# Kernel optimization log

Measured on AMD Instinct MI355X. Metric: run time of the kernel, lower is better.

## Reference

```python
import jax, jax.numpy as jnp
import numpy as np

ALPHA = 32.0
LN_EPS = 1e-5

def _cdist(a, b):
    # a: [C, M, K], b: [C, N, K] -> [C, M, N] euclidean distances
    d2 = (jnp.sum(a * a, -1)[:, :, None]
          + jnp.sum(b * b, -1)[:, None, :]
          - 2.0 * jnp.einsum('cmk,cnk->cmn', a, b))
    return jnp.sqrt(jnp.maximum(d2, 1e-12))

def setup_inputs() -> dict:
    key = jax.random.key(0)
    k1, k2 = jax.random.split(key)
    B, D, H, W, C = 8, 16, 28, 28, 256
    CN, SS = 128, 28 * 28
    x = jax.random.normal(k1, (B, D, H, W, C), dtype=jnp.float32)
    ln_weight = jnp.ones((C,), dtype=jnp.float32)
    ln_bias = jnp.zeros((C,), dtype=jnp.float32)
    cluster_center = jax.random.uniform(k2, (C, CN, SS), dtype=jnp.float32)
    return {"x": x, "ln_weight": ln_weight, "ln_bias": ln_bias,
            "cluster_center": cluster_center}

def reference(x, ln_weight, ln_bias, cluster_center):
    B, D, H, W, C = x.shape
    CN = cluster_center.shape[1]
    # LayerNorm over last dim (feature_dim)
    mu = jnp.mean(x, -1, keepdims=True)
    var = jnp.mean(jnp.square(x - mu), -1, keepdims=True)
    xn = (x - mu) * jax.lax.rsqrt(var + LN_EPS) * ln_weight + ln_bias
    # B D H W C -> C (B D) (H W)
    x_re = jnp.transpose(xn, (4, 0, 1, 2, 3)).reshape(C, B * D, H * W)
    soft_assign = _cdist(x_re, cluster_center)          # [C, B*D, CN]
    # C (B D) CN -> B D C CN
    x_distance = jnp.transpose(soft_assign.reshape(C, B, D, CN), (1, 2, 0, 3))
    # NegSoftAssign: exp(-alpha*(x - min)) normalized == softmax(-alpha*x)
    x_distance_assign = jax.nn.softmax(-ALPHA * x_distance, axis=-1)
    cluster_dist = _cdist(cluster_center, cluster_center)  # [C, CN, CN]
    return (x_distance, x_distance_assign, cluster_dist)
```

## Files before the change

### kernel.cpp

```cpp
#include <hip/hip_runtime.h>
#include <hip/hip_bf16.h>
#include <math.h>

#define C_DIM 256
#define BD    128
#define HW    784
#define CN    128
#define KPAD  832
#define KTILES 26

typedef short bf16x8 __attribute__((ext_vector_type(8)));
typedef float f32x4 __attribute__((ext_vector_type(4)));

__device__ inline ushort f2b(float f) {
  unsigned u = __float_as_uint(f);
  unsigned r = (u + 0x7FFFu + ((u >> 16) & 1u)) >> 16;
  return (ushort)r;
}

__global__ __launch_bounds__(256, 4) void prep_kernel(
    const float* __restrict__ x, const float* __restrict__ lnw,
    const float* __restrict__ lnb, const float* __restrict__ cc,
    ushort* __restrict__ xre, ushort* __restrict__ ccb) {
  __shared__ __align__(16) ushort btile[256 * 64];
  const int t = threadIdx.x, bid = blockIdx.x;
  const int w = t >> 6, lane = t & 63;
  const int q = lane >> 4, l = lane & 15;

  if (bid < 2048) {
    const int c = bid >> 3;
    const int r = (bid & 7) * 16 + w * 4 + q;
    const float4* src = (const float4*)(cc + ((size_t)c * CN + r) * HW);
    ushort* dst = ccb + ((size_t)c * CN + r) * KPAD;
    float4 v[13];
#pragma unroll
    for (int i = 0; i < 13; ++i) {
      if (i < 12 || l < 4) v[i] = src[i * 16 + l];
    }
#pragma unroll
    for (int i = 0; i < 13; ++i) {
      if (i < 12 || l < 4) {
        ushort4 o;
        o.x = f2b(v[i].x); o.y = f2b(v[i].y);
        o.z = f2b(v[i].z); o.w = f2b(v[i].w);
        *(ushort4*)(dst + (i * 16 + l) * 4) = o;
      }
    }
    if (l < 12) *(ushort4*)(dst + 784 + l * 4) = make_ushort4(0, 0, 0, 0);
    return;
  }

  const int idx = bid - 2048;
  const int bx = idx % 13;
  const int bd = idx / 13;
  const int hw0 = bx * 64;
  const bool last = (bx == 12);
  const int ngroups = last ? 1 : 4;
  const int rpw = ngroups * 4;
  const int xr2 = (l & 12) | ((l & 3) << 4);
  if (last) {
    int xf = ((t >> 2) & 12) ^ ((t & 12) << 2);
    for (int r = 16; r < 64; r += 4)
      *(ushort4*)&btile[t * 64 + (r ^ xf)] = make_ushort4(0, 0, 0, 0);
  }
  float4 wv[4], bv[4];
#pragma unroll
  for (int s = 0; s < 4; ++s) {
    wv[s] = *(const float4*)(lnw + s * 64 + l * 4);
    bv[s] = *(const float4*)(lnb + s * 64 + l * 4);
  }
  const float* xb = x + ((size_t)bd * HW + hw0) * 256 + l * 4;

#define LOADG(V, g)                                                            \
  do {                                                                         \
    int r_ = w * rpw + (g) * 4 + q;                                            \
    _Pragma("unroll") for (int s = 0; s < 4; ++s)                              \
        V[s] = *(const float4*)(xb + (size_t)r_ * 256 + s * 64);               \
  } while (0)

#define PROC(V, g)                                                             \
  do {                                                                         \
    int r_ = w * rpw + (g) * 4 + q;                                            \
    float sum = 0.f, sq = 0.f;                                                 \
    _Pragma("unroll") for (int s = 0; s < 4; ++s) {                            \
      sum += V[s].x + V[s].y + V[s].z + V[s].w;                                \
      sq = fmaf(V[s].x, V[s].x, sq); sq = fmaf(V[s].y, V[s].y, sq);            \
      sq = fmaf(V[s].z, V[s].z, sq); sq = fmaf(V[s].w, V[s].w, sq);            \
    }                                                                          \
    for (int off = 1; off <= 8; off <<= 1) {                                   \
      sum += __shfl_xor(sum, off, 64);                                         \
      sq  += __shfl_xor(sq, off, 64);                                          \
    }                                                                          \
    float mu = sum * (1.f / 256.f);                                            \
    float var = fmaf(-mu, mu, sq * (1.f / 256.f));                             \
    float sc = rsqrtf(var + 1e-5f);                                            \
    int rp_ = r_ ^ xr2;                                                        \
    _Pragma("unroll") for (int s = 0; s < 4; ++s) {                            \
      float y0 = (V[s].x - mu) * sc * wv[s].x + bv[s].x;                       \
      float y1 = (V[s].y - mu) * sc * wv[s].y + bv[s].y;                       \
      float y2 = (V[s].z - mu) * sc * wv[s].z + bv[s].z;                       \
      float y3 = (V[s].w - mu) * sc * wv[s].w + bv[s].w;                       \
      int c_ = s * 64 + l * 4;                                                 \
      btile[(c_ + 0) * 64 + rp_] = f2b(y0);                                    \
      btile[(c_ + 1) * 64 + rp_] = f2b(y1);                                    \
      btile[(c_ + 2) * 64 + rp_] = f2b(y2);                                    \
      btile[(c_ + 3) * 64 + rp_] = f2b(y3);                                    \
    }                                                                          \
  } while (0)

  float4 va[4], vb[4];
  LOADG(va, 0);
  if (ngroups > 1) {
    LOADG(vb, 1);
    PROC(va, 0);
    LOADG(va, 2);
    PROC(vb, 1);
    LOADG(vb, 3);
    PROC(va, 2);
    PROC(vb, 3);
  } else {
    PROC(va, 0);
  }
#undef LOADG
#undef PROC
  __syncthreads();
#pragma unroll
  for (int i = 0; i < 16; ++i) {
    int c = w * 64 + i * 4 + (lane >> 4);
    int xw = ((c >> 2) & 12) ^ ((c & 12) << 2);
    int ho = (lane & 15) * 4;
    uint2 val = *(const uint2*)&btile[c * 64 + (ho ^ xw)];
    *(uint2*)(xre + (size_t)c * (BD * KPAD) + (size_t)bd * KPAD + hw0 + ho) = val;
  }
}

__global__ __launch_bounds__(512) void gemm_fused_kernel(
    const ushort* __restrict__ xre, const ushort* __restrict__ ccb,
    float* __restrict__ out_d, float* __restrict__ out_s,
    float* __restrict__ out_c) {
  __shared__ __align__(16) ushort At[2][4096];
  __shared__ __align__(16) ushort Bt[2][4096];
  __shared__ float an_l[128], bn_l[128];
  const int c = blockIdx.x;
  const int t = threadIdx.x, w = t >> 6, lane = t & 63;
  const int quad = lane >> 4, ln = lane & 15;
  const ushort* Ag = xre + (size_t)c * (128 * KPAD);
  const ushort* Bg = ccb + (size_t)c * (128 * KPAD);

  f32x4 accx[8], accc[8];
  f32x4 accd = f32x4{0.f, 0.f, 0.f, 0.f};
  for (int j = 0; j < 8; ++j) {
    accx[j] = f32x4{0.f, 0.f, 0.f, 0.f};
    accc[j] = f32x4{0.f, 0.f, 0.f, 0.f};
  }

  const int srow = t >> 2, scq = (t & 3) ^ (srow & 3);
  const ushort* gA = Ag + (size_t)srow * KPAD + scq * 8;
  const ushort* gB = Bg + (size_t)srow * KPAD + scq * 8;

  const int m = w * 16 + ln;
  const int aoff = (m * 4 + (quad ^ (m & 3))) * 8;
  int boff[8];
#pragma unroll
  for (int j = 0; j < 8; ++j) {
    int n = j * 16 + ln;
    boff[j] = (n * 4 + (quad ^ (n & 3))) * 8;
  }

#define ISSUE(k, p)                                                            \
  do {                                                                         \
    int kb = (k) * 32;                                                         \
    __builtin_amdgcn_global_load_lds(                                          \
        (const __attribute__((address_space(1))) unsigned int*)(gA + kb),      \
        (__attribute__((address_space(3))) unsigned int*)&At[p][t * 8], 16, 0, 0); \
    __builtin_amdgcn_global_load_lds(                                          \
        (const __attribute__((address_space(1))) unsigned int*)(gB + kb),      \
        (__attribute__((address_space(3))) unsigned int*)&Bt[p][t * 8], 16, 0, 0); \
  } while (0)

  ISSUE(0, 0);
  for (int k0 = 0; k0 < KTILES; ++k0) {
    __syncthreads();
    if (k0 < KTILES - 1) ISSUE(k0 + 1, (k0 + 1) & 1);
    const int p = k0 & 1;
    bf16x8 af = *(const bf16x8*)&At[p][aoff];
    bf16x8 ar = *(const bf16x8*)&Bt[p][aoff];
    accd = __builtin_amdgcn_mfma_f32_16x16x32_bf16(af, af, accd, 0, 0, 0);
#pragma unroll
    for (int j = 0; j < 8; ++j) {
      bf16x8 bfj = *(const bf16x8*)&Bt[p][boff[j]];
      accx[j] = __builtin_amdgcn_mfma_f32_16x16x32_bf16(af, bfj, accx[j], 0, 0, 0);
      accc[j] = __builtin_amdgcn_mfma_f32_16x16x32_bf16(ar, bfj, accc[j], 0, 0, 0);
    }
  }
#undef ISSUE

  if ((ln >> 2) == quad) {
    an_l[w * 16 + ln] = accd[ln & 3];
    bn_l[w * 16 + ln] = accc[w][ln & 3];
  }
  __syncthreads();

  float cn[8];
  for (int j = 0; j < 8; ++j) cn[j] = bn_l[j * 16 + ln];
  float rx[4], rc[4];
  for (int r = 0; r < 4; ++r) {
    int p16 = quad * 4 + r;
    rx[r] = an_l[w * 16 + p16];
    rc[r] = bn_l[w * 16 + p16];
  }
  for (int r = 0; r < 4; ++r) {
    int mr = w * 16 + quad * 4 + r;
    float* ob = out_c + (size_t)c * (128 * 128) + (size_t)mr * 128;
    for (int j = 0; j < 8; ++j) {
      float d2 = rc[r] + cn[j] - 2.f * accc[j][r];
      ob[j * 16 + ln] = sqrtf(fmaxf(d2, 1e-12f));
    }
  }
  for (int r = 0; r < 4; ++r) {
    int mr = w * 16 + quad * 4 + r;
    float dr[8];
    for (int j = 0; j < 8; ++j) {
      float d2 = rx[r] + cn[j] - 2.f * accx[j][r];
      dr[j] = sqrtf(fmaxf(d2, 1e-12f));
    }
    float* ob = out_d + ((size_t)mr * 256 + c) * 128;
    for (int j = 0; j < 8; ++j) ob[j * 16 + ln] = dr[j];
    float mn = dr[0];
    for (int j = 1; j < 8; ++j) mn = fminf(mn, dr[j]);
    for (int off = 1; off <= 8; off <<= 1) mn = fminf(mn, __shfl_xor(mn, off, 64));
    float e[8], s = 0.f;
    for (int j = 0; j < 8; ++j) { e[j] = __expf(-32.f * (dr[j] - mn)); s += e[j]; }
    for (int off = 1; off <= 8; off <<= 1) s += __shfl_xor(s, off, 64);
    float inv = 1.f / s;
    float* os = out_s + ((size_t)mr * 256 + c) * 128;
    for (int j = 0; j < 8; ++j) os[j * 16 + ln] = e[j] * inv;
  }
}

extern "C" void kernel_launch(void* const* d_in, const int* in_sizes, int n_in,
                              void* d_out, int out_size, void* d_ws, size_t ws_size,
                              hipStream_t stream) {
  const float* x   = (const float*)d_in[0];
  const float* lnw = (const float*)d_in[1];
  const float* lnb = (const float*)d_in[2];
  const float* cc  = (const float*)d_in[3];
  float* out   = (float*)d_out;
  float* out_d = out;
  float* out_s = out + 4194304;
  float* out_c = out + 8388608;

  ushort* xre_b = (ushort*)d_ws;
  ushort* cc_b  = xre_b + 27262976;

  prep_kernel<<<3712, 256, 0, stream>>>(x, lnw, lnb, cc, xre_b, cc_b);
  gemm_fused_kernel<<<256, 512, 0, stream>>>(xre_b, cc_b, out_d, out_s, out_c);
}
```

Measured before the change: 288.4 us.

## Split GEMM blocks per channel by row halves, shrink prep tiles, XCD-aware mapping

The fused GEMM now launches two 256-thread blocks per channel instead of one 512-thread block. Each block computes one 64-row half of the x-vs-center product and the matching half of the center-center distances, and also computes the other half's center norms locally. Blocks are mapped so that consecutive channels sit on the same XCD. The prep kernel processes 32-row hw tiles instead of 64, with smaller LDS, a dedicated zero-padding block, and higher occupancy. The aim is more blocks for better CU utilisation. The cost is redundant B-tile loads and extra norm MFMAs per block.

```diff
diff --git a/kernel.cpp b/kernel.cpp
--- a/kernel.cpp
+++ b/kernel.cpp
@@ -8,6 +8,7 @@
 #define CN    128
 #define KPAD  832
 #define KTILES 26
+#define CC_BLOCKS 2048
 
 typedef short bf16x8 __attribute__((ext_vector_type(8)));
 typedef float f32x4 __attribute__((ext_vector_type(4)));
@@ -18,16 +19,16 @@
   return (ushort)r;
 }
 
-__global__ __launch_bounds__(256, 4) void prep_kernel(
+__global__ __launch_bounds__(256, 5) void prep_kernel(
     const float* __restrict__ x, const float* __restrict__ lnw,
     const float* __restrict__ lnb, const float* __restrict__ cc,
     ushort* __restrict__ xre, ushort* __restrict__ ccb) {
-  __shared__ __align__(16) ushort btile[256 * 64];
+  __shared__ __align__(16) ushort btile[256 * 32];
   const int t = threadIdx.x, bid = blockIdx.x;
   const int w = t >> 6, lane = t & 63;
   const int q = lane >> 4, l = lane & 15;
 
-  if (bid < 2048) {
+  if (bid < CC_BLOCKS) {
     const int c = bid >> 3;
     const int r = (bid & 7) * 16 + w * 4 + q;
     const float4* src = (const float4*)(cc + ((size_t)c * CN + r) * HW);
@@ -50,19 +51,36 @@
     return;
   }
 
-  const int idx = bid - 2048;
-  const int bx = idx % 13;
-  const int bd = idx / 13;
-  const int hw0 = bx * 64;
-  const bool last = (bx == 12);
-  const int ngroups = last ? 1 : 4;
+  const int idx = bid - CC_BLOCKS;
+  const int bx = idx % 26;
+  const int bd = idx / 26;
+  const int hw0 = bx * 32;
+
+  if (bx == 25) {
+#pragma unroll
+    for (int i = 0; i < 8; ++i) {
+      int c = w * 64 + i * 8 + (lane >> 3);
+      int ho = (lane & 7) * 4;
+      *(uint2*)(xre + (size_t)c * (BD * KPAD) + (size_t)bd * KPAD + hw0 + ho) =
+          make_uint2(0u, 0u);
+    }
+    return;
+  }
+
+  const bool half = (bx == 24);
+  const int ngroups = half ? 1 : 2;
   const int rpw = ngroups * 4;
-  const int xr2 = (l & 12) | ((l & 3) << 4);
-  if (last) {
-    int xf = ((t >> 2) & 12) ^ ((t & 12) << 2);
-    for (int r = 16; r < 64; r += 4)
-      *(ushort4*)&btile[t * 64 + (r ^ xf)] = make_ushort4(0, 0, 0, 0);
-  }
+  const int msk = (l & 7) << 2;
+
+  if (half) {
+    int rp2 = (16 + w * 4 + q) ^ msk;
+#pragma unroll
+    for (int s = 0; s < 4; ++s)
+#pragma unroll
+      for (int j = 0; j < 4; ++j)
+        btile[(s * 64 + l * 4 + j) * 32 + rp2] = 0;
+  }
+
   float4 wv[4], bv[4];
 #pragma unroll
   for (int s = 0; s < 4; ++s) {
@@ -94,17 +112,17 @@
     float mu = sum * (1.f / 256.f);                                            \
     float var = fmaf(-mu, mu, sq * (1.f / 256.f));                             \
     float sc = rsqrtf(var + 1e-5f);                                            \
-    int rp_ = r_ ^ xr2;                                                        \
+    int rp_ = r_ ^ msk;                                                        \
     _Pragma("unroll") for (int s = 0; s < 4; ++s) {                            \
       float y0 = (V[s].x - mu) * sc * wv[s].x + bv[s].x;                       \
       float y1 = (V[s].y - mu) * sc * wv[s].y + bv[s].y;                       \
       float y2 = (V[s].z - mu) * sc * wv[s].z + bv[s].z;                       \
       float y3 = (V[s].w - mu) * sc * wv[s].w + bv[s].w;                       \
       int c_ = s * 64 + l * 4;                                                 \
-      btile[(c_ + 0) * 64 + rp_] = f2b(y0);                                    \
-      btile[(c_ + 1) * 64 + rp_] = f2b(y1);                                    \
-      btile[(c_ + 2) * 64 + rp_] = f2b(y2);                                    \
-      btile[(c_ + 3) * 64 + rp_] = f2b(y3);                                    \
+      btile[(c_ + 0) * 32 + rp_] = f2b(y0);                                    \
+      btile[(c_ + 1) * 32 + rp_] = f2b(y1);                                    \
+      btile[(c_ + 2) * 32 + rp_] = f2b(y2);                                    \
+      btile[(c_ + 3) * 32 + rp_] = f2b(y3);                                    \
     }                                                                          \
   } while (0)
 
@@ -113,11 +131,7 @@
   if (ngroups > 1) {
     LOADG(vb, 1);
     PROC(va, 0);
-    LOADG(va, 2);
     PROC(vb, 1);
-    LOADG(vb, 3);
-    PROC(va, 2);
-    PROC(vb, 3);
   } else {
     PROC(va, 0);
   }
@@ -125,41 +139,50 @@
 #undef PROC
   __syncthreads();
 #pragma unroll
-  for (int i = 0; i < 16; ++i) {
-    int c = w * 64 + i * 4 + (lane >> 4);
-    int xw = ((c >> 2) & 12) ^ ((c & 12) << 2);
-    int ho = (lane & 15) * 4;
-    uint2 val = *(const uint2*)&btile[c * 64 + (ho ^ xw)];
+  for (int i = 0; i < 8; ++i) {
+    int c = w * 64 + i * 8 + (lane >> 3);
+    int xw = ((c >> 2) & 7) << 2;
+    int ho = (lane & 7) * 4;
+    uint2 val = *(const uint2*)&btile[c * 32 + (ho ^ xw)];
     *(uint2*)(xre + (size_t)c * (BD * KPAD) + (size_t)bd * KPAD + hw0 + ho) = val;
   }
 }
 
-__global__ __launch_bounds__(512) void gemm_fused_kernel(
+__global__ __launch_bounds__(256, 2) void gemm_fused_kernel(
     const ushort* __restrict__ xre, const ushort* __restrict__ ccb,
     float* __restrict__ out_d, float* __restrict__ out_s,
     float* __restrict__ out_c) {
-  __shared__ __align__(16) ushort At[2][4096];
+  __shared__ __align__(16) ushort At[2][2048];
   __shared__ __align__(16) ushort Bt[2][4096];
-  __shared__ float an_l[128], bn_l[128];
-  const int c = blockIdx.x;
+  __shared__ float an_l[64], bn_l[128];
+  const int bid = blockIdx.x;
+  const int xcd = bid & 7, i6 = bid >> 3;
+  const int c = xcd * 32 + (i6 >> 1);
+  const int h = i6 & 1;
   const int t = threadIdx.x, w = t >> 6, lane = t & 63;
   const int quad = lane >> 4, ln = lane & 15;
-  const ushort* Ag = xre + (size_t)c * (128 * KPAD);
+  const ushort* Ag = xre + (size_t)c * (128 * KPAD) + (size_t)(h * 64) * KPAD;
   const ushort* Bg = ccb + (size_t)c * (128 * KPAD);
 
   f32x4 accx[8], accc[8];
-  f32x4 accd = f32x4{0.f, 0.f, 0.f, 0.f};
+  f32x4 accd  = f32x4{0.f, 0.f, 0.f, 0.f};
+  f32x4 accbd = f32x4{0.f, 0.f, 0.f, 0.f};
+#pragma unroll
   for (int j = 0; j < 8; ++j) {
     accx[j] = f32x4{0.f, 0.f, 0.f, 0.f};
     accc[j] = f32x4{0.f, 0.f, 0.f, 0.f};
   }
 
   const int srow = t >> 2, scq = (t & 3) ^ (srow & 3);
-  const ushort* gA = Ag + (size_t)srow * KPAD + scq * 8;
-  const ushort* gB = Bg + (size_t)srow * KPAD + scq * 8;
+  const ushort* gA  = Ag + (size_t)srow * KPAD + scq * 8;
+  const ushort* gB1 = Bg + (size_t)srow * KPAD + scq * 8;
+  const ushort* gB2 = Bg + (size_t)(srow + 64) * KPAD + scq * 8;
 
   const int m = w * 16 + ln;
-  const int aoff = (m * 4 + (quad ^ (m & 3))) * 8;
+  const int aoff  = (m * 4 + (quad ^ (m & 3))) * 8;
+  const int aroff = ((h * 64 + m) * 4 + (quad ^ (m & 3))) * 8;
+  const int nD = (1 - h) * 64 + w * 16 + ln;
+  const int bdoff = (nD * 4 + (quad ^ (nD & 3))) * 8;
   int boff[8];
 #pragma unroll
   for (int j = 0; j < 8; ++j) {
@@ -174,8 +197,11 @@
         (const __attribute__((address_space(1))) unsigned int*)(gA + kb),      \
         (__attribute__((address_space(3))) unsigned int*)&At[p][t * 8], 16, 0, 0); \
     __builtin_amdgcn_global_load_lds(                                          \
-        (const __attribute__((address_space(1))) unsigned int*)(gB + kb),      \
+        (const __attribute__((address_space(1))) unsigned int*)(gB1 + kb),     \
         (__attribute__((address_space(3))) unsigned int*)&Bt[p][t * 8], 16, 0, 0); \
+    __builtin_amdgcn_global_load_lds(                                          \
+        (const __attribute__((address_space(1))) unsigned int*)(gB2 + kb),     \
+        (__attribute__((address_space(3))) unsigned int*)&Bt[p][t * 8 + 2048], 16, 0, 0); \
   } while (0)
 
   ISSUE(0, 0);
@@ -183,9 +209,11 @@
     __syncthreads();
     if (k0 < KTILES - 1) ISSUE(k0 + 1, (k0 + 1) & 1);
     const int p = k0 & 1;
-    bf16x8 af = *(const bf16x8*)&At[p][aoff];
-    bf16x8 ar = *(const bf16x8*)&Bt[p][aoff];
-    accd = __builtin_amdgcn_mfma_f32_16x16x32_bf16(af, af, accd, 0, 0, 0);
+    bf16x8 af  = *(const bf16x8*)&At[p][aoff];
+    bf16x8 ar  = *(const bf16x8*)&Bt[p][aroff];
+    bf16x8 bdr = *(const bf16x8*)&Bt[p][bdoff];
+    accd  = __builtin_amdgcn_mfma_f32_16x16x32_bf16(af, af, accd, 0, 0, 0);
+    accbd = __builtin_amdgcn_mfma_f32_16x16x32_bf16(bdr, bdr, accbd, 0, 0, 0);
 #pragma unroll
     for (int j = 0; j < 8; ++j) {
       bf16x8 bfj = *(const bf16x8*)&Bt[p][boff[j]];
@@ -196,44 +224,65 @@
 #undef ISSUE
 
   if ((ln >> 2) == quad) {
-    an_l[w * 16 + ln] = accd[ln & 3];
-    bn_l[w * 16 + ln] = accc[w][ln & 3];
+#pragma unroll
+    for (int r2 = 0; r2 < 4; ++r2)
+      if (r2 == (ln & 3)) {
+        an_l[w * 16 + ln] = accd[r2];
+        bn_l[(1 - h) * 64 + w * 16 + ln] = accbd[r2];
+      }
+#pragma unroll
+    for (int j = 0; j < 8; ++j)
+      if (j == h * 4 + w) {
+#pragma unroll
+        for (int r2 = 0; r2 < 4; ++r2)
+          if (r2 == (ln & 3))
+            bn_l[h * 64 + w * 16 + ln] = accc[j][r2];
+      }
   }
   __syncthreads();
 
   float cn[8];
+#pragma unroll
   for (int j = 0; j < 8; ++j) cn[j] = bn_l[j * 16 + ln];
   float rx[4], rc[4];
+#pragma unroll
   for (int r = 0; r < 4; ++r) {
-    int p16 = quad * 4 + r;
-    rx[r] = an_l[w * 16 + p16];
-    rc[r] = bn_l[w * 16 + p16];
-  }
+    rx[r] = an_l[w * 16 + quad * 4 + r];
+    rc[r] = bn_l[h * 64 + w * 16 + quad * 4 + r];
+  }
+#pragma unroll
   for (int r = 0; r < 4; ++r) {
-    int mr = w * 16 + quad * 4 + r;
+    int mr = h * 64 + w * 16 + quad * 4 + r;
     float* ob = out_c + (size_t)c * (128 * 128) + (size_t)mr * 128;
+#pragma unroll
     for (int j = 0; j < 8; ++j) {
       float d2 = rc[r] + cn[j] - 2.f * accc[j][r];
       ob[j * 16 + ln] = sqrtf(fmaxf(d2, 1e-12f));
     }
   }
+#pragma unroll
   for (int r = 0; r < 4; ++r) {
-    int mr = w * 16 + quad * 4 + r;
+    int mr = h * 64 + w * 16 + quad * 4 + r;
     float dr[8];
+#pragma unroll
     for (int j = 0; j < 8; ++j) {
       float d2 = rx[r] + cn[j] - 2.f * accx[j][r];
       dr[j] = sqrtf(fmaxf(d2, 1e-12f));
     }
     float* ob = out_d + ((size_t)mr * 256 + c) * 128;
+#pragma unroll
     for (int j = 0; j < 8; ++j) ob[j * 16 + ln] = dr[j];
     float mn = dr[0];
+#pragma unroll
     for (int j = 1; j < 8; ++j) mn = fminf(mn, dr[j]);
     for (int off = 1; off <= 8; off <<= 1) mn = fminf(mn, __shfl_xor(mn, off, 64));
     float e[8], s = 0.f;
+#pragma unroll
     for (int j = 0; j < 8; ++j) { e[j] = __expf(-32.f * (dr[j] - mn)); s += e[j]; }
     for (int off = 1; off <= 8; off <<= 1) s += __shfl_xor(s, off, 64);
     float inv = 1.f / s;
     float* os = out_s + ((size_t)mr * 256 + c) * 128;
+#pragma unroll
     for (int j = 0; j < 8; ++j) os[j * 16 + ln] = e[j] * inv;
   }
 }
@@ -253,6 +302,6 @@
   ushort* xre_b = (ushort*)d_ws;
   ushort* cc_b  = xre_b + 27262976;
 
-  prep_kernel<<<3712, 256, 0, stream>>>(x, lnw, lnb, cc, xre_b, cc_b);
-  gemm_fused_kernel<<<256, 512, 0, stream>>>(xre_b, cc_b, out_d, out_s, out_c);
+  prep_kernel<<<5376, 256, 0, stream>>>(x, lnw, lnb, cc, xre_b, cc_b);
+  gemm_fused_kernel<<<512, 256, 0, stream>>>(xre_b, cc_b, out_d, out_s, out_c);
 }
```

After: 306.0 us. 6.1% more time.
